# Kernel optimization log

Measured on AMD Instinct MI355X. Metric: run time of the kernel, lower is better.

## Reference

```python
import jax, jax.numpy as jnp
import numpy as np

N_NODES = 100000
N_EDGES = 1600000
F_IN, NH1, NH2, NH3, N_CLS = 128, 64, 18, 9, 10
KS = [8, 6, 4, 4]
BN_EPS = 1e-5


def setup_inputs() -> dict:
    key = jax.random.key(0)
    ks = jax.random.split(key, 32)
    inp = {
        "x": jax.random.normal(ks[0], (N_NODES, F_IN), dtype=jnp.float32),
        "edge_index": jax.random.randint(ks[1], (2, N_EDGES), 0, N_NODES, dtype=jnp.int32),
    }
    dims = [(F_IN, NH1), (NH1, NH2), (NH2, NH3), (NH3, N_CLS)]
    for i, ((din, dout), K) in enumerate(zip(dims, KS), start=1):
        scale = 1.0 / np.sqrt(din * K)
        inp[f"W{i}"] = jax.random.normal(ks[2 * i], (K, din, dout), dtype=jnp.float32) * scale
        inp[f"b{i}"] = jnp.zeros((dout,), dtype=jnp.float32)
    for i, d in enumerate([NH1, NH2, NH3], start=1):
        inp[f"bn{i}_g"] = jnp.ones((d,), dtype=jnp.float32)
        inp[f"bn{i}_b"] = jnp.zeros((d,), dtype=jnp.float32)
        inp[f"bn{i}_m"] = jnp.zeros((d,), dtype=jnp.float32)
        inp[f"bn{i}_v"] = jnp.ones((d,), dtype=jnp.float32)
    return inp


def _cheb_conv(x, W, b, src, dst, w_norm, n_nodes):
    # PyG ChebConv with lambda_max=2: L_hat = -D^{-1/2} A D^{-1/2}
    def prop(t):  # L_hat @ t via edge scatter
        return jax.ops.segment_sum(w_norm[:, None] * t[src], dst, num_segments=n_nodes)

    K = W.shape[0]
    Tx0 = x
    out = Tx0 @ W[0]
    Tx1 = prop(Tx0)
    out = out + Tx1 @ W[1]
    for k in range(2, K):
        Tx2 = 2.0 * prop(Tx1) - Tx0
        out = out + Tx2 @ W[k]
        Tx0, Tx1 = Tx1, Tx2
    return out + b


def _bn_eval(x, g, b, m, v):
    return (x - m) * (g * jax.lax.rsqrt(v + BN_EPS)) + b


def reference(x, edge_index, W1, b1, W2, b2, W3, b3, W4, b4,
              bn1_g, bn1_b, bn1_m, bn1_v,
              bn2_g, bn2_b, bn2_m, bn2_v,
              bn3_g, bn3_b, bn3_m, bn3_v):
    n = x.shape[0]
    src, dst = edge_index[0], edge_index[1]
    ones = jnp.ones((src.shape[0],), dtype=x.dtype)
    deg = jax.ops.segment_sum(ones, dst, num_segments=n)
    dinv = jnp.where(deg > 0, jax.lax.rsqrt(jnp.maximum(deg, 1.0)), 0.0)
    w_norm = -dinv[src] * dinv[dst]

    h = jax.nn.relu(_bn_eval(_cheb_conv(x, W1, b1, src, dst, w_norm, n), bn1_g, bn1_b, bn1_m, bn1_v))
    h = jax.nn.relu(_bn_eval(_cheb_conv(h, W2, b2, src, dst, w_norm, n), bn2_g, bn2_b, bn2_m, bn2_v))
    h = jax.nn.relu(_bn_eval(_cheb_conv(h, W3, b3, src, dst, w_norm, n), bn3_g, bn3_b, bn3_m, bn3_v))
    return _cheb_conv(h, W4, b4, src, dst, w_norm, n)
```

## Files before the change

kernel.cpp:

```cpp
#include <hip/hip_runtime.h>

#define NN 100000
#define NE 1600000
#define BN_EPS 1e-5f

typedef _Float16 half1;
typedef _Float16 half4 __attribute__((ext_vector_type(4)));
typedef _Float16 h8 __attribute__((ext_vector_type(8)));
typedef float f4 __attribute__((ext_vector_type(4)));
typedef float f8 __attribute__((ext_vector_type(8)));

static inline int divup(int a, int b) { return (a + b - 1) / b; }


__global__ void hist_kernel(const int* __restrict__ dst, int* __restrict__ deg, int e) {
    int i = blockIdx.x * blockDim.x + threadIdx.x;
    if (i < e) atomicAdd(&deg[dst[i]], 1);
}

__global__ void blksum_kernel(const int* __restrict__ deg, int* __restrict__ blk, int n) {
    __shared__ int red[256];
    int t = threadIdx.x;
    int base = blockIdx.x * 1024 + t * 4;
    int s = 0;
#pragma unroll
    for (int i = 0; i < 4; ++i) {
        int idx = base + i;
        if (idx < n) s += deg[idx];
    }
    red[t] = s;
    __syncthreads();
    for (int off = 128; off > 0; off >>= 1) {
        if (t < off) red[t] += red[t + off];
        __syncthreads();
    }
    if (t == 0) blk[blockIdx.x] = red[0];
}

__global__ void blkscan_kernel(int* __restrict__ blk, int nb, int* __restrict__ row_ptr, int n) {
    __shared__ int sh[256];
    int t = threadIdx.x;
    int v = (t < nb) ? blk[t] : 0;
    sh[t] = v;
    __syncthreads();
    for (int off = 1; off < 256; off <<= 1) {
        int u = (t >= off) ? sh[t - off] : 0;
        __syncthreads();
        sh[t] += u;
        __syncthreads();
    }
    if (t < nb) blk[t] = (t == 0) ? 0 : sh[t - 1];
    if (t == nb - 1) row_ptr[n] = sh[t];
}

__global__ void emit_kernel(const int* __restrict__ deg, const int* __restrict__ blk,
                            int* __restrict__ row_ptr, int n) {
    __shared__ int red[256];
    int t = threadIdx.x;
    int base = blockIdx.x * 1024 + t * 4;
    int d[4];
    int s = 0;
#pragma unroll
    for (int i = 0; i < 4; ++i) {
        int idx = base + i;
        d[i] = (idx < n) ? deg[idx] : 0;
        s += d[i];
    }
    red[t] = s;
    __syncthreads();
    for (int off = 1; off < 256; off <<= 1) {
        int u = (t >= off) ? red[t - off] : 0;
        __syncthreads();
        red[t] += u;
        __syncthreads();
    }
    int run = blk[blockIdx.x] + ((t == 0) ? 0 : red[t - 1]);
#pragma unroll
    for (int i = 0; i < 4; ++i) {
        int idx = base + i;
        if (idx < n) { row_ptr[idx] = run; run += d[i]; }
    }
}

__global__ void dinv_kernel(const int* __restrict__ deg, float* __restrict__ dinv, int n) {
    int i = blockIdx.x * blockDim.x + threadIdx.x;
    if (i < n) {
        int d = deg[i];
        dinv[i] = (d > 0) ? rsqrtf((float)d) : 0.f;
    }
}

__global__ void scatter_kernel(const int* __restrict__ src, const int* __restrict__ dst,
                               const int* __restrict__ row_ptr, int* __restrict__ cursor,
                               const float* __restrict__ dinv,
                               int2* __restrict__ cw, int e) {
    int i = blockIdx.x * blockDim.x + threadIdx.x;
    if (i >= e) return;
    int s = src[i], d = dst[i];
    int pos = row_ptr[d] + atomicAdd(&cursor[d], 1);
    unsigned long long packed =
        (unsigned int)s | ((unsigned long long)(unsigned int)__float_as_int(-dinv[s] * dinv[d]) << 32);
    __builtin_nontemporal_store(packed, (unsigned long long*)&cw[pos]);
}


__global__ void cvtx_kernel(const float4* __restrict__ X, half4* __restrict__ Xh, int tot4) {
    int i = blockIdx.x * blockDim.x + threadIdx.x;
    if (i >= tot4) return;
    float4 v = X[i];
    half4 h;
    h.x = (half1)v.x; h.y = (half1)v.y; h.z = (half1)v.z; h.w = (half1)v.w;
    Xh[i] = h;
}

__global__ void transw_kernel(const float* __restrict__ W, half1* __restrict__ Wt) {
    int i = blockIdx.x * blockDim.x + threadIdx.x;
    if (i >= 512 * 128) return;
    int kd = i >> 9;
    int og = i & 511;
    int k = og >> 6, o = og & 63;
    Wt[(size_t)og * 128 + kd] = (half1)W[((size_t)k * 128 + kd) * 64 + o];
}

__global__ void padw_kernel(const float* __restrict__ src, float* __restrict__ dst,
                            int K, int dins, int douts, int dind, int doutd) {
    int i = blockIdx.x * blockDim.x + threadIdx.x;
    int tot = K * dind * doutd;
    if (i >= tot) return;
    int o = i % doutd;
    int r = i / doutd;
    int dd = r % dind;
    int k = r / dind;
    dst[i] = (dd < dins && o < douts) ? src[((size_t)k * dins + dd) * douts + o] : 0.f;
}

__global__ void proph8_kernel(const h8* __restrict__ feat, const h8* __restrict__ sub,
                              const h8* __restrict__ add, h8* __restrict__ outh,
                              f8* __restrict__ outf,
                              const int* __restrict__ row_ptr, const int2* __restrict__ cw,
                              int n, float scale, int has_sub, int bnrelu,
                              const float* __restrict__ bn_g, const float* __restrict__ bn_b,
                              const float* __restrict__ bn_m, const float* __restrict__ bn_v) {
    int idx = blockIdx.x * blockDim.x + threadIdx.x;
    if (idx >= n * 8) return;
    int nd = idx >> 3;
    int f = idx & 7;
    int e0 = row_ptr[nd], e1 = row_ptr[nd + 1];
    f8 a0 = {0.f, 0.f, 0.f, 0.f, 0.f, 0.f, 0.f, 0.f}, a1 = a0, a2 = a0, a3 = a0;
    int e = e0;
    for (; e + 4 <= e1; e += 4) {
        int2 q0 = cw[e], q1 = cw[e + 1], q2 = cw[e + 2], q3 = cw[e + 3];
        f8 v0 = __builtin_convertvector(feat[(size_t)q0.x * 8 + f], f8);
        f8 v1 = __builtin_convertvector(feat[(size_t)q1.x * 8 + f], f8);
        f8 v2 = __builtin_convertvector(feat[(size_t)q2.x * 8 + f], f8);
        f8 v3 = __builtin_convertvector(feat[(size_t)q3.x * 8 + f], f8);
        a0 += __int_as_float(q0.y) * v0;
        a1 += __int_as_float(q1.y) * v1;
        a2 += __int_as_float(q2.y) * v2;
        a3 += __int_as_float(q3.y) * v3;
    }
    for (; e < e1; ++e) {
        int2 q = cw[e];
        a0 += __int_as_float(q.y) * __builtin_convertvector(feat[(size_t)q.x * 8 + f], f8);
    }
    f8 r = ((a0 + a1) + (a2 + a3)) * scale;
    if (has_sub) r -= __builtin_convertvector(sub[idx], f8);
    r += __builtin_convertvector(add[idx], f8);
    if (bnrelu) {
#pragma unroll
        for (int c = 0; c < 8; ++c) {
            int o = f * 8 + c;
            float sc = bn_g[o] * rsqrtf(bn_v[o] + BN_EPS);
            r[c] = fmaxf(fmaf(r[c] - bn_m[o], sc, bn_b[o]), 0.f);
        }
    }
    if (outf) {
        outf[idx] = r;
    } else {
        outh[idx] = __builtin_convertvector(r, h8);
    }
}

__global__ void proph_kernel(const half4* __restrict__ feat, const half4* __restrict__ sub,
                             const half4* __restrict__ add, half4* __restrict__ outh,
                             f4* __restrict__ outf,
                             const int* __restrict__ row_ptr, const int2* __restrict__ cw,
                             int n, int dim4, float scale, int has_sub,
                             int bnrelu, int used,
                             const float* __restrict__ bn_g, const float* __restrict__ bn_b,
                             const float* __restrict__ bn_m, const float* __restrict__ bn_v) {
    int idx = blockIdx.x * blockDim.x + threadIdx.x;
    if (idx >= n * dim4) return;
    int nd = idx / dim4;
    int f = idx - nd * dim4;
    int e0 = row_ptr[nd], e1 = row_ptr[nd + 1];
    f4 a0 = {0.f, 0.f, 0.f, 0.f}, a1 = a0, a2 = a0, a3 = a0;
    int e = e0;
    for (; e + 4 <= e1; e += 4) {
        int2 q0 = cw[e], q1 = cw[e + 1], q2 = cw[e + 2], q3 = cw[e + 3];
        f4 v0 = __builtin_convertvector(feat[(size_t)q0.x * dim4 + f], f4);
        f4 v1 = __builtin_convertvector(feat[(size_t)q1.x * dim4 + f], f4);
        f4 v2 = __builtin_convertvector(feat[(size_t)q2.x * dim4 + f], f4);
        f4 v3 = __builtin_convertvector(feat[(size_t)q3.x * dim4 + f], f4);
        a0 += __int_as_float(q0.y) * v0;
        a1 += __int_as_float(q1.y) * v1;
        a2 += __int_as_float(q2.y) * v2;
        a3 += __int_as_float(q3.y) * v3;
    }
    for (; e < e1; ++e) {
        int2 q = cw[e];
        a0 += __int_as_float(q.y) * __builtin_convertvector(feat[(size_t)q.x * dim4 + f], f4);
    }
    f4 r = ((a0 + a1) + (a2 + a3)) * scale;
    if (has_sub) r -= __builtin_convertvector(sub[idx], f4);
    r += __builtin_convertvector(add[idx], f4);
    if (bnrelu) {
#pragma unroll
        for (int c = 0; c < 4; ++c) {
            int o = f * 4 + c;
            if (o < used) {
                float sc = bn_g[o] * rsqrtf(bn_v[o] + BN_EPS);
                r[c] = fmaxf(fmaf(r[c] - bn_m[o], sc, bn_b[o]), 0.f);
            } else r[c] = 0.f;
        }
    }
    if (outf) {
        outf[idx] = r;
    } else {
        half4 h;
        h.x = (half1)r.x; h.y = (half1)r.y; h.z = (half1)r.z; h.w = (half1)r.w;
        outh[idx] = h;
    }
}

__global__ void propl_kernel(const half4* __restrict__ feat, const half4* __restrict__ sub,
                             const half4* __restrict__ add, float* __restrict__ out,
                             const int* __restrict__ row_ptr, const int2* __restrict__ cw,
                             int n) {
    int idx = blockIdx.x * blockDim.x + threadIdx.x;
    if (idx >= n * 3) return;
    int nd = idx / 3;
    int f = idx - nd * 3;
    int e0 = row_ptr[nd], e1 = row_ptr[nd + 1];
    f4 a0 = {0.f, 0.f, 0.f, 0.f}, a1 = a0, a2 = a0, a3 = a0;
    int e = e0;
    for (; e + 4 <= e1; e += 4) {
        int2 q0 = cw[e], q1 = cw[e + 1], q2 = cw[e + 2], q3 = cw[e + 3];
        a0 += __int_as_float(q0.y) * __builtin_convertvector(feat[(size_t)q0.x * 3 + f], f4);
        a1 += __int_as_float(q1.y) * __builtin_convertvector(feat[(size_t)q1.x * 3 + f], f4);
        a2 += __int_as_float(q2.y) * __builtin_convertvector(feat[(size_t)q2.x * 3 + f], f4);
        a3 += __int_as_float(q3.y) * __builtin_convertvector(feat[(size_t)q3.x * 3 + f], f4);
    }
    for (; e < e1; ++e) {
        int2 q = cw[e];
        a0 += __int_as_float(q.y) * __builtin_convertvector(feat[(size_t)q.x * 3 + f], f4);
    }
    f4 r = (a0 + a1) + (a2 + a3);
    r -= __builtin_convertvector(sub[idx], f4);
    r += __builtin_convertvector(add[idx], f4);
    int o = f * 4;
    float* orow = out + (size_t)nd * 10;
    if (o + 0 < 10) orow[o + 0] = r.x;
    if (o + 1 < 10) orow[o + 1] = r.y;
    if (o + 2 < 10) orow[o + 2] = r.z;
    if (o + 3 < 10) orow[o + 3] = r.w;
}

__global__ __launch_bounds__(256) void gemm_mfma_kernel(
        const half1* __restrict__ Xh, const half1* __restrict__ Wt,
        const float* __restrict__ bias, half1* __restrict__ CB, int n) {
    int lane = threadIdx.x & 63;
    int wave = threadIdx.x >> 6;
    int m16 = lane & 15;
    int quad = lane >> 4;
    int ks = blockIdx.y * 4 + wave;
    int ntile = blockIdx.x * 64;

    f4 acc[4][4];
#pragma unroll
    for (int nt = 0; nt < 4; ++nt)
#pragma unroll
        for (int i = 0; i < 4; ++i) acc[nt][i] = (f4){0.f, 0.f, 0.f, 0.f};

#pragma unroll
    for (int kc = 0; kc < 4; ++kc) {
        int koff = kc * 32 + quad * 8;
        h8 a[4];
#pragma unroll
        for (int i = 0; i < 4; ++i)
            a[i] = *(const h8*)(Wt + (size_t)(ks * 64 + i * 16 + m16) * 128 + koff);
        h8 b[4];
#pragma unroll
        for (int nt = 0; nt < 4; ++nt) {
            int node = min(ntile + nt * 16 + m16, n - 1);
            b[nt] = *(const h8*)(Xh + (size_t)node * 128 + koff);
        }
#pragma unroll
        for (int nt = 0; nt < 4; ++nt)
#pragma unroll
            for (int i = 0; i < 4; ++i)
                acc[nt][i] = __builtin_amdgcn_mfma_f32_16x16x32_f16(a[i], b[nt], acc[nt][i], 0, 0, 0);
    }

#pragma unroll
    for (int nt = 0; nt < 4; ++nt) {
        int node = ntile + nt * 16 + m16;
        if (node < n) {
#pragma unroll
            for (int i = 0; i < 4; ++i) {
                int ob = i * 16 + quad * 4;
                f4 v = acc[nt][i];
                if (ks == 0) {
                    const f4 b4 = *(const f4*)(bias + ob);
                    v += b4;
                }
                half4 h;
                h.x = (half1)v[0]; h.y = (half1)v[1]; h.z = (half1)v[2]; h.w = (half1)v[3];
                *(half4*)(CB + ((size_t)ks * n + node) * 64 + ob) = h;
            }
        }
    }
}

template <int KK, int DIN4, int NACC>
__global__ void gemm_smallw_kernel(const float* __restrict__ X, const float* __restrict__ Wp,
                                   const float* __restrict__ bias, int dout,
                                   half4* __restrict__ CB, int n) {
    int lane = threadIdx.x & 63;
    int k = __builtin_amdgcn_readfirstlane((int)(threadIdx.x >> 6));
    int node0 = blockIdx.x * 64 + lane;
    int node = min(node0, n - 1);
    f4 acc[NACC];
#pragma unroll
    for (int i = 0; i < NACC; ++i) {
        f4 v = {0.f, 0.f, 0.f, 0.f};
        if (k == 0 && bias) {
#pragma unroll
            for (int c = 0; c < 4; ++c) {
                int o = i * 4 + c;
                v[c] = (o < dout) ? bias[o] : 0.f;
            }
        }
        acc[i] = v;
    }
    const f4* Xr = (const f4*)(X + (size_t)node * (DIN4 * 4));
    const f4* Wk = (const f4*)(Wp + (size_t)k * (DIN4 * 4) * (NACC * 4));
    for (int d4 = 0; d4 < DIN4; ++d4) {
        f4 xv = Xr[d4];
#pragma unroll
        for (int j = 0; j < 4; ++j) {
            float xs = xv[j];
#pragma unroll
            for (int i = 0; i < NACC; ++i)
                acc[i] += xs * Wk[(d4 * 4 + j) * NACC + i];
        }
    }
    if (node0 < n) {
        size_t base = ((size_t)k * n + node) * NACC;
#pragma unroll
        for (int i = 0; i < NACC; ++i) {
            half4 h;
            h.x = (half1)acc[i].x; h.y = (half1)acc[i].y;
            h.z = (half1)acc[i].z; h.w = (half1)acc[i].w;
            CB[base + i] = h;
        }
    }
}


extern "C" void kernel_launch(void* const* d_in, const int* in_sizes, int n_in,
                              void* d_out, int out_size, void* d_ws, size_t ws_size,
                              hipStream_t stream) {
    const float* x  = (const float*)d_in[0];
    const int*   ei = (const int*)d_in[1];
    const float* Wl[4] = {(const float*)d_in[2], (const float*)d_in[4],
                          (const float*)d_in[6], (const float*)d_in[8]};
    const float* bl[4] = {(const float*)d_in[3], (const float*)d_in[5],
                          (const float*)d_in[7], (const float*)d_in[9]};
    const float* bn[3][4];
    for (int l = 0; l < 3; ++l)
        for (int j = 0; j < 4; ++j)
            bn[l][j] = (const float*)d_in[10 + 4 * l + j];

    char* ws = (char*)d_ws;
    size_t off = 0;
    auto alloc = [&](size_t bytes) -> void* {
        void* p = (void*)(ws + off);
        off = (off + bytes + 255) & ~(size_t)255;
        return p;
    };
    int*   deg     = (int*)alloc(NN * 4);
    int*   row_ptr = (int*)alloc((NN + 1) * 4);
    int*   cursor  = (int*)alloc(NN * 4);
    int*   blks    = (int*)alloc(128 * 4);
    float* dinv    = (float*)alloc(NN * 4);
    int2*  cw      = (int2*)alloc((size_t)NE * 8);
    half1* CB1h    = (half1*)alloc((size_t)8 * NN * 64 * 2);
    half1* CBsh    = (half1*)alloc((size_t)6 * NN * 20 * 2);
    half1* S0      = (half1*)alloc((size_t)NN * 64 * 2);
    half1* S1      = (half1*)alloc((size_t)NN * 64 * 2);
    half1* S2      = (half1*)alloc((size_t)NN * 64 * 2);
    float* H1f     = (float*)alloc((size_t)NN * 64 * 4);
    float* H2f     = (float*)alloc((size_t)NN * 20 * 4);
    float* H3f     = (float*)alloc((size_t)NN * 12 * 4);
    float* Wp2     = (float*)alloc((size_t)6 * 64 * 20 * 4);
    float* Wp3     = (float*)alloc((size_t)4 * 20 * 12 * 4);
    float* Wp4     = (float*)alloc((size_t)4 * 12 * 12 * 4);
    half1* Xh      = (half1*)alloc((size_t)NN * 128 * 2);
    half1* Wt1     = (half1*)alloc((size_t)512 * 128 * 2);

    const int* srcp = ei;
    const int* dstp = ei + NE;
    const int nscan = divup(NN, 1024);
    const int NB = divup(NN, 64);

    hipMemsetAsync(deg, 0, NN * 4, stream);
    hipMemsetAsync(cursor, 0, NN * 4, stream);
    hist_kernel<<<divup(NE, 256), 256, 0, stream>>>(dstp, deg, NE);
    blksum_kernel<<<nscan, 256, 0, stream>>>(deg, blks, NN);
    blkscan_kernel<<<1, 256, 0, stream>>>(blks, nscan, row_ptr, NN);
    emit_kernel<<<nscan, 256, 0, stream>>>(deg, blks, row_ptr, NN);
    dinv_kernel<<<divup(NN, 256), 256, 0, stream>>>(deg, dinv, NN);
    scatter_kernel<<<divup(NE, 256), 256, 0, stream>>>(srcp, dstp, row_ptr, cursor, dinv, cw, NE);

    cvtx_kernel<<<divup(NN * 32, 256), 256, 0, stream>>>((const float4*)x, (half4*)Xh, NN * 32);
    transw_kernel<<<divup(512 * 128, 256), 256, 0, stream>>>(Wl[0], Wt1);
    padw_kernel<<<divup(6 * 64 * 20, 256), 256, 0, stream>>>(Wl[1], Wp2, 6, 64, 18, 64, 20);
    padw_kernel<<<divup(4 * 20 * 12, 256), 256, 0, stream>>>(Wl[2], Wp3, 4, 18, 9, 20, 12);
    padw_kernel<<<divup(4 * 12 * 12, 256), 256, 0, stream>>>(Wl[3], Wp4, 4, 9, 10, 12, 12);

    auto prop1 = [&](const half1* feat, const half1* sub, const half1* add,
                     half1* outh, float* outf, float scale, int bnrelu,
                     const float* g, const float* bb, const float* m, const float* v) {
        proph8_kernel<<<divup(NN * 8, 256), 256, 0, stream>>>(
            (const h8*)feat, (const h8*)sub, (const h8*)add,
            (h8*)outh, (f8*)outf, row_ptr, cw, NN, scale,
            sub != nullptr, bnrelu, g, bb, m, v);
    };
    auto prop = [&](const half1* feat, const half1* sub, const half1* add,
                    half1* outh, float* outf, int dim4, float scale,
                    int bnrelu, int used, const float* g, const float* bb,
                    const float* m, const float* v) {
        proph_kernel<<<divup(NN * dim4, 256), 256, 0, stream>>>(
            (const half4*)feat, (const half4*)sub, (const half4*)add,
            (half4*)outh, (f4*)outf, row_ptr, cw, NN, dim4, scale,
            sub != nullptr, bnrelu, used, g, bb, m, v);
    };

    gemm_mfma_kernel<<<dim3(NB, 2), 256, 0, stream>>>(Xh, Wt1, bl[0], CB1h, NN);
    {
        auto C = [&](int k) { return (const half1*)(CB1h + (size_t)k * NN * 64); };
        prop1(C(7), nullptr, C(6), S0, nullptr, 2.f, 0, 0, 0, 0, 0);
        prop1(S0, C(7), C(5), S1, nullptr, 2.f, 0, 0, 0, 0, 0);
        prop1(S1, S0, C(4), S2, nullptr, 2.f, 0, 0, 0, 0, 0);
        prop1(S2, S1, C(3), S0, nullptr, 2.f, 0, 0, 0, 0, 0);
        prop1(S0, S2, C(2), S1, nullptr, 2.f, 0, 0, 0, 0, 0);
        prop1(S1, S0, C(1), S2, nullptr, 2.f, 0, 0, 0, 0, 0);
        prop1(S2, S1, C(0), nullptr, H1f, 1.f, 1,
              bn[0][0], bn[0][1], bn[0][2], bn[0][3]);
    }

    gemm_smallw_kernel<6, 16, 5><<<NB, 384, 0, stream>>>(H1f, Wp2, bl[1], 18,
                                                         (half4*)CBsh, NN);
    {
        auto C = [&](int k) { return (const half1*)(CBsh + (size_t)k * NN * 20); };
        prop(C(5), nullptr, C(4), S0, nullptr, 5, 2.f, 0, 18, 0, 0, 0, 0);
        prop(S0, C(5), C(3), S1, nullptr, 5, 2.f, 0, 18, 0, 0, 0, 0);
        prop(S1, S0, C(2), S2, nullptr, 5, 2.f, 0, 18, 0, 0, 0, 0);
        prop(S2, S1, C(1), S0, nullptr, 5, 2.f, 0, 18, 0, 0, 0, 0);
        prop(S0, S2, C(0), nullptr, H2f, 5, 1.f, 1, 18,
             bn[1][0], bn[1][1], bn[1][2], bn[1][3]);
    }

    gemm_smallw_kernel<4, 5, 3><<<NB, 256, 0, stream>>>(H2f, Wp3, bl[2], 9,
                                                        (half4*)CBsh, NN);
    {
        auto C = [&](int k) { return (const half1*)(CBsh + (size_t)k * NN * 12); };
        prop(C(3), nullptr, C(2), S0, nullptr, 3, 2.f, 0, 9, 0, 0, 0, 0);
        prop(S0, C(3), C(1), S1, nullptr, 3, 2.f, 0, 9, 0, 0, 0, 0);
        prop(S1, S0, C(0), nullptr, H3f, 3, 1.f, 1, 9,
             bn[2][0], bn[2][1], bn[2][2], bn[2][3]);
    }

    gemm_smallw_kernel<4, 3, 3><<<NB, 256, 0, stream>>>(H3f, Wp4, bl[3], 10,
                                                        (half4*)CBsh, NN);
    {
        auto C = [&](int k) { return (const half1*)(CBsh + (size_t)k * NN * 12); };
        prop(C(3), nullptr, C(2), S0, nullptr, 3, 2.f, 0, 10, 0, 0, 0, 0);
        prop(S0, C(3), C(1), S1, nullptr, 3, 2.f, 0, 10, 0, 0, 0, 0);
        propl_kernel<<<divup(NN * 3, 256), 256, 0, stream>>>(
            (const half4*)S1, (const half4*)S0, (const half4*)CBsh,
            (float*)d_out, row_ptr, cw, NN);
    }
}
```

Before: 883.4 us.

## Build CSR via two-level bucketed scatter and pack degree into edge words

Replaces the global-atomic cursor scatter with a per-chunk bucket histogram, a bucket offset pass, a shared-memory binned scatter into a temporary buffer, and a per-bucket finalize that writes CSR entries locally. Edge records shrink from 8 bytes to 4: the source index uses 17 bits and the source degree is packed into the upper bits. The normalization weight is recomputed in the propagation kernels with rsqrt from the packed degree and the row length. This is meant to cut the scattered global atomics and the edge-array bandwidth in every propagation, in exchange for extra rsqrt math per edge and more setup kernels. Degrees above 32767 are clamped, and the temporary buffer aliases a later workspace region.

```diff
diff --git a/kernel.cpp b/kernel.cpp
--- a/kernel.cpp
+++ b/kernel.cpp
@@ -3,6 +3,12 @@
 #define NN 100000
 #define NE 1600000
 #define BN_EPS 1e-5f
+
+#define BSH 7
+#define BSZ (1 << BSH)
+#define NBUCK 782
+#define NC 192
+#define CE 8334
 
 typedef _Float16 half1;
 typedef _Float16 half4 __attribute__((ext_vector_type(4)));
@@ -12,10 +18,26 @@
 
 static inline int divup(int a, int b) { return (a + b - 1) / b; }
 
-
-__global__ void hist_kernel(const int* __restrict__ dst, int* __restrict__ deg, int e) {
-    int i = blockIdx.x * blockDim.x + threadIdx.x;
-    if (i < e) atomicAdd(&deg[dst[i]], 1);
+__device__ __forceinline__ float wsrc(unsigned int q) {
+    unsigned int dg = q >> 17;
+    return dg ? rsqrtf((float)dg) : 0.f;
+}
+
+
+__global__ void hist2_kernel(const int* __restrict__ dst, int* __restrict__ deg,
+                             int* __restrict__ hist_g) {
+    __shared__ int h[NBUCK];
+    int c = blockIdx.x;
+    for (int i = threadIdx.x; i < NBUCK; i += blockDim.x) h[i] = 0;
+    __syncthreads();
+    int e0 = c * CE, e1 = min(e0 + CE, NE);
+    for (int e = e0 + threadIdx.x; e < e1; e += blockDim.x) {
+        int d = dst[e];
+        atomicAdd(&deg[d], 1);
+        atomicAdd(&h[d >> BSH], 1);
+    }
+    __syncthreads();
+    for (int i = threadIdx.x; i < NBUCK; i += blockDim.x) hist_g[c * NBUCK + i] = h[i];
 }
 
 __global__ void blksum_kernel(const int* __restrict__ deg, int* __restrict__ blk, int n) {
@@ -82,25 +104,55 @@
     }
 }
 
-__global__ void dinv_kernel(const int* __restrict__ deg, float* __restrict__ dinv, int n) {
-    int i = blockIdx.x * blockDim.x + threadIdx.x;
-    if (i < n) {
-        int d = deg[i];
-        dinv[i] = (d > 0) ? rsqrtf((float)d) : 0.f;
-    }
-}
-
-__global__ void scatter_kernel(const int* __restrict__ src, const int* __restrict__ dst,
-                               const int* __restrict__ row_ptr, int* __restrict__ cursor,
-                               const float* __restrict__ dinv,
-                               int2* __restrict__ cw, int e) {
-    int i = blockIdx.x * blockDim.x + threadIdx.x;
-    if (i >= e) return;
-    int s = src[i], d = dst[i];
-    int pos = row_ptr[d] + atomicAdd(&cursor[d], 1);
-    unsigned long long packed =
-        (unsigned int)s | ((unsigned long long)(unsigned int)__float_as_int(-dinv[s] * dinv[d]) << 32);
-    __builtin_nontemporal_store(packed, (unsigned long long*)&cw[pos]);
+__global__ void bucketoff_kernel(const int* __restrict__ row_ptr, const int* __restrict__ hist_g,
+                                 int* __restrict__ off_g) {
+    int b = blockIdx.x * blockDim.x + threadIdx.x;
+    if (b >= NBUCK) return;
+    int run = row_ptr[b << BSH];
+#pragma unroll 4
+    for (int c = 0; c < NC; ++c) {
+        off_g[c * NBUCK + b] = run;
+        run += hist_g[c * NBUCK + b];
+    }
+}
+
+__global__ void binscatter_kernel(const int* __restrict__ src, const int* __restrict__ dst,
+                                  const int* __restrict__ deg, const int* __restrict__ off_g,
+                                  int2* __restrict__ tmp) {
+    __shared__ int off_l[NBUCK];
+    int myx = blockIdx.x & 7;
+    int c = blockIdx.x >> 3;
+    for (int i = threadIdx.x; i < NBUCK; i += blockDim.x)
+        off_l[i] = ((i & 7) == myx) ? off_g[c * NBUCK + i] : 0;
+    __syncthreads();
+    int e0 = c * CE, e1 = min(e0 + CE, NE);
+    for (int e = e0 + threadIdx.x; e < e1; e += blockDim.x) {
+        int d = dst[e];
+        int b = d >> BSH;
+        if ((b & 7) != myx) continue;
+        int s = src[e];
+        int dg = deg[s];
+        if (dg > 32767) dg = 32767;
+        int pos = atomicAdd(&off_l[b], 1);
+        tmp[pos] = make_int2(s | (dg << 17), d & (BSZ - 1));
+    }
+}
+
+__global__ void finalize_kernel(const int2* __restrict__ tmp, const int* __restrict__ row_ptr,
+                                unsigned int* __restrict__ cw) {
+    __shared__ int cnt[BSZ];
+    int b = blockIdx.x;
+    for (int i = threadIdx.x; i < BSZ; i += blockDim.x) cnt[i] = 0;
+    __syncthreads();
+    int base = b << BSH;
+    int e0 = row_ptr[base];
+    int e1 = row_ptr[min(base + BSZ, NN)];
+    for (int e = e0 + threadIdx.x; e < e1; e += blockDim.x) {
+        int2 r = tmp[e];
+        int d = base + r.y;
+        int k = atomicAdd(&cnt[r.y], 1);
+        cw[row_ptr[d] + k] = (unsigned int)r.x;
+    }
 }
 
 
@@ -137,7 +189,7 @@
 __global__ void proph8_kernel(const h8* __restrict__ feat, const h8* __restrict__ sub,
                               const h8* __restrict__ add, h8* __restrict__ outh,
                               f8* __restrict__ outf,
-                              const int* __restrict__ row_ptr, const int2* __restrict__ cw,
+                              const int* __restrict__ row_ptr, const unsigned int* __restrict__ cw,
                               int n, float scale, int has_sub, int bnrelu,
                               const float* __restrict__ bn_g, const float* __restrict__ bn_b,
                               const float* __restrict__ bn_m, const float* __restrict__ bn_v) {
@@ -149,21 +201,23 @@
     f8 a0 = {0.f, 0.f, 0.f, 0.f, 0.f, 0.f, 0.f, 0.f}, a1 = a0, a2 = a0, a3 = a0;
     int e = e0;
     for (; e + 4 <= e1; e += 4) {
-        int2 q0 = cw[e], q1 = cw[e + 1], q2 = cw[e + 2], q3 = cw[e + 3];
-        f8 v0 = __builtin_convertvector(feat[(size_t)q0.x * 8 + f], f8);
-        f8 v1 = __builtin_convertvector(feat[(size_t)q1.x * 8 + f], f8);
-        f8 v2 = __builtin_convertvector(feat[(size_t)q2.x * 8 + f], f8);
-        f8 v3 = __builtin_convertvector(feat[(size_t)q3.x * 8 + f], f8);
-        a0 += __int_as_float(q0.y) * v0;
-        a1 += __int_as_float(q1.y) * v1;
-        a2 += __int_as_float(q2.y) * v2;
-        a3 += __int_as_float(q3.y) * v3;
+        unsigned int q0 = cw[e], q1 = cw[e + 1], q2 = cw[e + 2], q3 = cw[e + 3];
+        f8 v0 = __builtin_convertvector(feat[(size_t)(q0 & 0x1FFFFu) * 8 + f], f8);
+        f8 v1 = __builtin_convertvector(feat[(size_t)(q1 & 0x1FFFFu) * 8 + f], f8);
+        f8 v2 = __builtin_convertvector(feat[(size_t)(q2 & 0x1FFFFu) * 8 + f], f8);
+        f8 v3 = __builtin_convertvector(feat[(size_t)(q3 & 0x1FFFFu) * 8 + f], f8);
+        a0 += wsrc(q0) * v0;
+        a1 += wsrc(q1) * v1;
+        a2 += wsrc(q2) * v2;
+        a3 += wsrc(q3) * v3;
     }
     for (; e < e1; ++e) {
-        int2 q = cw[e];
-        a0 += __int_as_float(q.y) * __builtin_convertvector(feat[(size_t)q.x * 8 + f], f8);
-    }
-    f8 r = ((a0 + a1) + (a2 + a3)) * scale;
+        unsigned int q = cw[e];
+        a0 += wsrc(q) * __builtin_convertvector(feat[(size_t)(q & 0x1FFFFu) * 8 + f], f8);
+    }
+    int degd = e1 - e0;
+    float ms = (degd > 0) ? -scale * rsqrtf((float)degd) : 0.f;
+    f8 r = ((a0 + a1) + (a2 + a3)) * ms;
     if (has_sub) r -= __builtin_convertvector(sub[idx], f8);
     r += __builtin_convertvector(add[idx], f8);
     if (bnrelu) {
@@ -184,7 +238,7 @@
 __global__ void proph_kernel(const half4* __restrict__ feat, const half4* __restrict__ sub,
                              const half4* __restrict__ add, half4* __restrict__ outh,
                              f4* __restrict__ outf,
-                             const int* __restrict__ row_ptr, const int2* __restrict__ cw,
+                             const int* __restrict__ row_ptr, const unsigned int* __restrict__ cw,
                              int n, int dim4, float scale, int has_sub,
                              int bnrelu, int used,
                              const float* __restrict__ bn_g, const float* __restrict__ bn_b,
@@ -197,21 +251,23 @@
     f4 a0 = {0.f, 0.f, 0.f, 0.f}, a1 = a0, a2 = a0, a3 = a0;
     int e = e0;
     for (; e + 4 <= e1; e += 4) {
-        int2 q0 = cw[e], q1 = cw[e + 1], q2 = cw[e + 2], q3 = cw[e + 3];
-        f4 v0 = __builtin_convertvector(feat[(size_t)q0.x * dim4 + f], f4);
-        f4 v1 = __builtin_convertvector(feat[(size_t)q1.x * dim4 + f], f4);
-        f4 v2 = __builtin_convertvector(feat[(size_t)q2.x * dim4 + f], f4);
-        f4 v3 = __builtin_convertvector(feat[(size_t)q3.x * dim4 + f], f4);
-        a0 += __int_as_float(q0.y) * v0;
-        a1 += __int_as_float(q1.y) * v1;
-        a2 += __int_as_float(q2.y) * v2;
-        a3 += __int_as_float(q3.y) * v3;
+        unsigned int q0 = cw[e], q1 = cw[e + 1], q2 = cw[e + 2], q3 = cw[e + 3];
+        f4 v0 = __builtin_convertvector(feat[(size_t)(q0 & 0x1FFFFu) * dim4 + f], f4);
+        f4 v1 = __builtin_convertvector(feat[(size_t)(q1 & 0x1FFFFu) * dim4 + f], f4);
+        f4 v2 = __builtin_convertvector(feat[(size_t)(q2 & 0x1FFFFu) * dim4 + f], f4);
+        f4 v3 = __builtin_convertvector(feat[(size_t)(q3 & 0x1FFFFu) * dim4 + f], f4);
+        a0 += wsrc(q0) * v0;
+        a1 += wsrc(q1) * v1;
+        a2 += wsrc(q2) * v2;
+        a3 += wsrc(q3) * v3;
     }
     for (; e < e1; ++e) {
-        int2 q = cw[e];
-        a0 += __int_as_float(q.y) * __builtin_convertvector(feat[(size_t)q.x * dim4 + f], f4);
-    }
-    f4 r = ((a0 + a1) + (a2 + a3)) * scale;
+        unsigned int q = cw[e];
+        a0 += wsrc(q) * __builtin_convertvector(feat[(size_t)(q & 0x1FFFFu) * dim4 + f], f4);
+    }
+    int degd = e1 - e0;
+    float ms = (degd > 0) ? -scale * rsqrtf((float)degd) : 0.f;
+    f4 r = ((a0 + a1) + (a2 + a3)) * ms;
     if (has_sub) r -= __builtin_convertvector(sub[idx], f4);
     r += __builtin_convertvector(add[idx], f4);
     if (bnrelu) {
@@ -235,7 +291,7 @@
 
 __global__ void propl_kernel(const half4* __restrict__ feat, const half4* __restrict__ sub,
                              const half4* __restrict__ add, float* __restrict__ out,
-                             const int* __restrict__ row_ptr, const int2* __restrict__ cw,
+                             const int* __restrict__ row_ptr, const unsigned int* __restrict__ cw,
                              int n) {
     int idx = blockIdx.x * blockDim.x + threadIdx.x;
     if (idx >= n * 3) return;
@@ -245,17 +301,19 @@
     f4 a0 = {0.f, 0.f, 0.f, 0.f}, a1 = a0, a2 = a0, a3 = a0;
     int e = e0;
     for (; e + 4 <= e1; e += 4) {
-        int2 q0 = cw[e], q1 = cw[e + 1], q2 = cw[e + 2], q3 = cw[e + 3];
-        a0 += __int_as_float(q0.y) * __builtin_convertvector(feat[(size_t)q0.x * 3 + f], f4);
-        a1 += __int_as_float(q1.y) * __builtin_convertvector(feat[(size_t)q1.x * 3 + f], f4);
-        a2 += __int_as_float(q2.y) * __builtin_convertvector(feat[(size_t)q2.x * 3 + f], f4);
-        a3 += __int_as_float(q3.y) * __builtin_convertvector(feat[(size_t)q3.x * 3 + f], f4);
+        unsigned int q0 = cw[e], q1 = cw[e + 1], q2 = cw[e + 2], q3 = cw[e + 3];
+        a0 += wsrc(q0) * __builtin_convertvector(feat[(size_t)(q0 & 0x1FFFFu) * 3 + f], f4);
+        a1 += wsrc(q1) * __builtin_convertvector(feat[(size_t)(q1 & 0x1FFFFu) * 3 + f], f4);
+        a2 += wsrc(q2) * __builtin_convertvector(feat[(size_t)(q2 & 0x1FFFFu) * 3 + f], f4);
+        a3 += wsrc(q3) * __builtin_convertvector(feat[(size_t)(q3 & 0x1FFFFu) * 3 + f], f4);
     }
     for (; e < e1; ++e) {
-        int2 q = cw[e];
-        a0 += __int_as_float(q.y) * __builtin_convertvector(feat[(size_t)q.x * 3 + f], f4);
-    }
-    f4 r = (a0 + a1) + (a2 + a3);
+        unsigned int q = cw[e];
+        a0 += wsrc(q) * __builtin_convertvector(feat[(size_t)(q & 0x1FFFFu) * 3 + f], f4);
+    }
+    int degd = e1 - e0;
+    float ms = (degd > 0) ? -rsqrtf((float)degd) : 0.f;
+    f4 r = ((a0 + a1) + (a2 + a3)) * ms;
     r -= __builtin_convertvector(sub[idx], f4);
     r += __builtin_convertvector(add[idx], f4);
     int o = f * 4;
@@ -391,10 +449,8 @@
     };
     int*   deg     = (int*)alloc(NN * 4);
     int*   row_ptr = (int*)alloc((NN + 1) * 4);
-    int*   cursor  = (int*)alloc(NN * 4);
     int*   blks    = (int*)alloc(128 * 4);
-    float* dinv    = (float*)alloc(NN * 4);
-    int2*  cw      = (int2*)alloc((size_t)NE * 8);
+    unsigned int* cw = (unsigned int*)alloc((size_t)NE * 4);
     half1* CB1h    = (half1*)alloc((size_t)8 * NN * 64 * 2);
     half1* CBsh    = (half1*)alloc((size_t)6 * NN * 20 * 2);
     half1* S0      = (half1*)alloc((size_t)NN * 64 * 2);
@@ -409,19 +465,23 @@
     half1* Xh      = (half1*)alloc((size_t)NN * 128 * 2);
     half1* Wt1     = (half1*)alloc((size_t)512 * 128 * 2);
 
+    int2* tmp    = (int2*)CB1h;
+    int*  hist_g = (int*)((char*)CB1h + (16u << 20));
+    int*  off_g  = hist_g + NC * NBUCK;
+
     const int* srcp = ei;
     const int* dstp = ei + NE;
     const int nscan = divup(NN, 1024);
     const int NB = divup(NN, 64);
 
     hipMemsetAsync(deg, 0, NN * 4, stream);
-    hipMemsetAsync(cursor, 0, NN * 4, stream);
-    hist_kernel<<<divup(NE, 256), 256, 0, stream>>>(dstp, deg, NE);
+    hist2_kernel<<<NC, 256, 0, stream>>>(dstp, deg, hist_g);
     blksum_kernel<<<nscan, 256, 0, stream>>>(deg, blks, NN);
     blkscan_kernel<<<1, 256, 0, stream>>>(blks, nscan, row_ptr, NN);
     emit_kernel<<<nscan, 256, 0, stream>>>(deg, blks, row_ptr, NN);
-    dinv_kernel<<<divup(NN, 256), 256, 0, stream>>>(deg, dinv, NN);
-    scatter_kernel<<<divup(NE, 256), 256, 0, stream>>>(srcp, dstp, row_ptr, cursor, dinv, cw, NE);
+    bucketoff_kernel<<<divup(NBUCK, 256), 256, 0, stream>>>(row_ptr, hist_g, off_g);
+    binscatter_kernel<<<NC * 8, 256, 0, stream>>>(srcp, dstp, deg, off_g, tmp);
+    finalize_kernel<<<NBUCK, 256, 0, stream>>>(tmp, row_ptr, cw);
 
     cvtx_kernel<<<divup(NN * 32, 256), 256, 0, stream>>>((const float4*)x, (half4*)Xh, NN * 32);
     transw_kernel<<<divup(512 * 128, 256), 256, 0, stream>>>(Wl[0], Wt1);
```

New measurement: 856.2 us. 1.03x faster.
